# Performance work log

Hardware: AMD Instinct MI355X
Metric: run time of the kernel (lower is better)

The kernel has to match this reference:

```python
import jax, jax.numpy as jnp
import numpy as np


def setup_inputs() -> dict:
    key = jax.random.key(0)
    k1, k2 = jax.random.split(key)
    x = jax.random.normal(k1, (32, 64, 32, 32), dtype=jnp.float32)
    codebook = jax.random.normal(k2, (2048, 64), dtype=jnp.float32)
    return {"x": x, "codebook": codebook}


def reference(x, codebook):
    B, C, H, W = x.shape
    # (B, C, H, W) -> (B*H*W, C) channels-last flatten
    xf = jnp.transpose(x, (0, 2, 3, 1)).reshape(-1, C)
    d2 = (jnp.sum(xf * xf, axis=-1, keepdims=True)
          + jnp.sum(codebook * codebook, axis=-1)[None, :]
          - 2.0 * jnp.einsum('nc,kc->nk', xf, codebook))
    idx = jnp.argmin(d2, axis=-1)            # (B*H*W,)
    quant = codebook[idx]                    # (B*H*W, C)
    commitment_loss = jnp.mean((jax.lax.stop_gradient(quant) - xf) ** 2)
    codebook_loss = jnp.mean((quant - jax.lax.stop_gradient(xf)) ** 2)
    # Straight-through estimator
    quant_ste = xf + jax.lax.stop_gradient(quant - xf)
    quant_out = jnp.transpose(quant_ste.reshape(B, H, W, C), (0, 3, 1, 2))
    min_encoding_indices = idx.reshape(B, H, W)
    return quant_out, codebook_loss, commitment_loss, min_encoding_indices
```

## Files before the change

kernel.cpp:

```cpp
#include <hip/hip_runtime.h>

#define NROWS    32768
#define KENT     2048
#define OUT_Q_SZ 2097152
#define N_ELEMS  2097152.0f
#define THRG     1e-4f
#define KLO      0.0009765625f

typedef _Float16 f16x8  __attribute__((ext_vector_type(8)));
typedef float    f32x16 __attribute__((ext_vector_type(16)));

#define WS_EN    1024
#define WS_ENH   9216
#define WS_LIST  20480
#define WS_CBH   262144
#define WS_CBL   524288

__global__ __launch_bounds__(256) void vq_prep_kernel(
    const float* __restrict__ cb, float* __restrict__ ws)
{
    const int unit = blockIdx.x * 256 + threadIdx.x;
    if (unit == 0) { ws[0] = 0.0f; ((unsigned*)ws)[1] = 0u; ((unsigned*)ws)[2] = 0u; }

    const int gm = unit >> 8, ks = (unit >> 6) & 3, l = unit & 63;
    const int e  = gm * 32 + (l & 31);
    const int ch = ks * 16 + ((l >> 5) << 3);
    float4 v0 = *(const float4*)(cb + e * 64 + ch);
    float4 v1 = *(const float4*)(cb + e * 64 + ch + 4);
    float vv[8] = {v0.x,v0.y,v0.z,v0.w, v1.x,v1.y,v1.z,v1.w};
    f16x8 h, lo;
#pragma unroll
    for (int j = 0; j < 8; ++j) {
        _Float16 hi = (_Float16)vv[j];
        float r = (vv[j] - (float)hi) * 1024.0f;
        h[j] = hi; lo[j] = (_Float16)r;
    }
    *(f16x8*)((_Float16*)((char*)ws + WS_CBH) + (size_t)unit * 8) = h;
    *(f16x8*)((_Float16*)((char*)ws + WS_CBL) + (size_t)unit * 8) = lo;

    if (unit < KENT) {
        const float4* row = (const float4*)(cb + unit * 64);
        float s = 0.0f;
#pragma unroll
        for (int i = 0; i < 16; ++i) {
            float4 v = row[i];
            s += v.x * v.x + v.y * v.y + v.z * v.z + v.w * v.w;
        }
        *((float*)((char*)ws + WS_EN) + unit) = s;
        int ein = unit & 31;
        int half = (ein >> 2) & 1;
        int r = (ein & 3) + ((ein >> 3) << 2);
        *((float*)((char*)ws + WS_ENH) + (unit & ~31) + half * 16 + r) = -0.5f * s;
    }
}

__global__ __launch_bounds__(512, 4) void vq_main_kernel(
    const float* __restrict__ x, const float* __restrict__ cb,
    float* __restrict__ ws, float* __restrict__ out_q,
    float* __restrict__ out_idx)
{
    __shared__ float lds_x[64 * 68];
    __shared__ float enh_s[2048];
    __shared__ float mb1[64 * 4], mb2[64 * 4];
    __shared__ int   mbi[64 * 4];
    __shared__ int   idx_s[64], flag_s[64];
    __shared__ float wp[8];

    const _Float16* cbh  = (const _Float16*)((char*)ws + WS_CBH);
    const _Float16* cbl  = (const _Float16*)((char*)ws + WS_CBL);
    const float*    enhp = (const float*)((char*)ws + WS_ENH);
    unsigned* cnt  = (unsigned*)ws + 1;
    unsigned* list = (unsigned*)((char*)ws + WS_LIST);

    const int tid = threadIdx.x, bid = blockIdx.x;
    const int n0  = bid * 64;
    const int b   = n0 >> 10;
    const int hw0 = n0 & 1023;
    const float* xg = x + b * 65536 + hw0;

    {
        int c = tid >> 3, seg = tid & 7;
        float4 a0 = *(const float4*)(xg + c * 1024 + seg * 8);
        float4 a1 = *(const float4*)(xg + c * 1024 + seg * 8 + 4);
        *(float4*)(&lds_x[c * 68 + seg * 8])     = a0;
        *(float4*)(&lds_x[c * 68 + seg * 8 + 4]) = a1;
    }
#pragma unroll
    for (int i = tid; i < 2048; i += 512) enh_s[i] = enhp[i];
    __syncthreads();

    const int l   = tid & 63;
    const int wv  = tid >> 6;
    const int rgp = wv >> 2;
    const int eq  = wv & 3;
    const int r0  = rgp * 32;

    f16x8 bh[4], bl[4];
#pragma unroll
    for (int ks = 0; ks < 4; ++ks) {
        f16x8 h, lo;
#pragma unroll
        for (int j = 0; j < 8; ++j) {
            int ch = ks * 16 + ((l >> 5) << 3) + j;
            float f = lds_x[ch * 68 + r0 + (l & 31)];
            _Float16 hi = (_Float16)f;
            float r = (f - (float)hi) * 1024.0f;
            h[j] = hi; lo[j] = (_Float16)r;
        }
        bh[ks] = h; bl[ks] = lo;
    }

    float m1[4], m2[4]; int bx[4];
#pragma unroll
    for (int t = 0; t < 4; ++t) { m1[t] = -3.4e38f; m2[t] = -3.4e38f; bx[t] = 0; }

#pragma unroll 2
    for (int m = 0; m < 16; ++m) {
        const int gm = eq * 16 + m;
        const _Float16* ap = cbh + ((size_t)(gm * 4) * 64 + l) * 8;
        const _Float16* lp = cbl + ((size_t)(gm * 4) * 64 + l) * 8;
        f16x8 ah0 = *(const f16x8*)(ap);
        f16x8 ah1 = *(const f16x8*)(ap + 512);
        f16x8 ah2 = *(const f16x8*)(ap + 1024);
        f16x8 ah3 = *(const f16x8*)(ap + 1536);
        f16x8 al0 = *(const f16x8*)(lp);
        f16x8 al1 = *(const f16x8*)(lp + 512);
        f16x8 al2 = *(const f16x8*)(lp + 1024);
        f16x8 al3 = *(const f16x8*)(lp + 1536);

        f32x16 aA;
        {
            const float4* ep4 = (const float4*)(&enh_s[eq * 512 + m * 32 + ((l >> 5) << 4)]);
            float4 q0 = ep4[0], q1 = ep4[1], q2 = ep4[2], q3 = ep4[3];
            aA[0]=q0.x; aA[1]=q0.y; aA[2]=q0.z; aA[3]=q0.w;
            aA[4]=q1.x; aA[5]=q1.y; aA[6]=q1.z; aA[7]=q1.w;
            aA[8]=q2.x; aA[9]=q2.y; aA[10]=q2.z; aA[11]=q2.w;
            aA[12]=q3.x; aA[13]=q3.y; aA[14]=q3.z; aA[15]=q3.w;
        }
        f32x16 cA = {0.f,0.f,0.f,0.f,0.f,0.f,0.f,0.f,0.f,0.f,0.f,0.f,0.f,0.f,0.f,0.f};

        aA = __builtin_amdgcn_mfma_f32_32x32x16_f16(ah0, bh[0], aA, 0, 0, 0);
        cA = __builtin_amdgcn_mfma_f32_32x32x16_f16(ah0, bl[0], cA, 0, 0, 0);
        aA = __builtin_amdgcn_mfma_f32_32x32x16_f16(ah1, bh[1], aA, 0, 0, 0);
        cA = __builtin_amdgcn_mfma_f32_32x32x16_f16(ah1, bl[1], cA, 0, 0, 0);
        aA = __builtin_amdgcn_mfma_f32_32x32x16_f16(ah2, bh[2], aA, 0, 0, 0);
        cA = __builtin_amdgcn_mfma_f32_32x32x16_f16(ah2, bl[2], cA, 0, 0, 0);
        aA = __builtin_amdgcn_mfma_f32_32x32x16_f16(ah3, bh[3], aA, 0, 0, 0);
        cA = __builtin_amdgcn_mfma_f32_32x32x16_f16(ah3, bl[3], cA, 0, 0, 0);
        cA = __builtin_amdgcn_mfma_f32_32x32x16_f16(al0, bh[0], cA, 0, 0, 0);
        cA = __builtin_amdgcn_mfma_f32_32x32x16_f16(al1, bh[1], cA, 0, 0, 0);
        cA = __builtin_amdgcn_mfma_f32_32x32x16_f16(al2, bh[2], cA, 0, 0, 0);
        cA = __builtin_amdgcn_mfma_f32_32x32x16_f16(al3, bh[3], cA, 0, 0, 0);

        const int ebl = eq * 512 + m * 32 + ((l >> 5) << 2);
#pragma unroll
        for (int r = 0; r < 16; ++r) {
            int t = r >> 2;
            int ent = ebl + ((r >> 2) << 3) + (r & 3);
            float gA = fmaf(cA[r], KLO, aA[r]);
            bool  tA = gA > m1[t];
            m2[t] = __builtin_amdgcn_fmed3f(gA, m1[t], m2[t]);
            m1[t] = fmaxf(gA, m1[t]);
            bx[t] = tA ? ent : bx[t];
        }
    }

    {
        float v1 = m1[0], v2 = m2[0]; int ix = bx[0];
#pragma unroll
        for (int t = 1; t < 4; ++t) {
            bool gt = (m1[t] > v1) || (m1[t] == v1 && bx[t] < ix);
            float loser = gt ? v1 : m1[t];
            v1 = gt ? m1[t] : v1;
            ix = gt ? bx[t] : ix;
            v2 = fmaxf(loser, fmaxf(v2, m2[t]));
        }
        float o1 = __shfl_xor(v1, 32, 64);
        float o2 = __shfl_xor(v2, 32, 64);
        int   oi = __shfl_xor(ix, 32, 64);
        bool gt = (o1 > v1) || (o1 == v1 && oi < ix);
        float loser = gt ? v1 : o1;
        v1 = gt ? o1 : v1; ix = gt ? oi : ix;
        v2 = fmaxf(loser, fmaxf(v2, o2));
        if (l < 32) {
            int row = r0 + l;
            mb1[row * 4 + eq] = v1;
            mb2[row * 4 + eq] = v2;
            mbi[row * 4 + eq] = ix;
        }
    }
    __syncthreads();

    if (tid < 64) {
        float v1 = -3.4e38f, v2 = -3.4e38f; int ix = 0;
#pragma unroll
        for (int q = 0; q < 4; ++q) {
            float o1 = mb1[tid * 4 + q];
            float o2 = mb2[tid * 4 + q];
            int   oi = mbi[tid * 4 + q];
            bool gt = (o1 > v1) || (o1 == v1 && oi < ix);
            float loser = gt ? v1 : o1;
            v1 = gt ? o1 : v1; ix = gt ? oi : ix;
            v2 = fmaxf(loser, fmaxf(v2, o2));
        }
        out_idx[n0 + tid] = (float)ix;
        int fl = (v1 - v2) <= THRG;
        idx_s[tid] = ix; flag_s[tid] = fl;
        if (fl) { unsigned p = atomicAdd(cnt, 1u); list[p] = n0 + tid; }
    }
    __syncthreads();

    float lsum = 0.0f;
#pragma unroll
    for (int it = 0; it < 8; ++it) {
        int e = it * 512 + tid;
        int c = e >> 6, r = e & 63;
        float q  = cb[idx_s[r] * 64 + c];
        float xv = lds_x[c * 68 + r];
        out_q[(b << 16) + (c << 10) + hw0 + r] = xv + (q - xv);
        float df = q - xv;
        lsum += flag_s[r] ? 0.0f : df * df;
    }
#pragma unroll
    for (int mm = 1; mm < 64; mm <<= 1) lsum += __shfl_xor(lsum, mm, 64);
    if (l == 0) wp[wv] = lsum;
    __syncthreads();
    if (tid == 0) {
        float s = 0.0f;
#pragma unroll
        for (int w = 0; w < 8; ++w) s += wp[w];
        atomicAdd(ws, s);
    }
}

__global__ __launch_bounds__(256) void vq_fallback_kernel(
    const float* __restrict__ x, const float* __restrict__ cb,
    float* __restrict__ ws, float* __restrict__ out_q, float* __restrict__ out_idx)
{
    __shared__ float x_s[64];
    __shared__ float rd[256];
    __shared__ int   ri[256];
    __shared__ unsigned lastflag;

    const float* en = (const float*)((char*)ws + WS_EN);
    const unsigned F = *(const unsigned*)((char*)ws + 4);
    const unsigned* list = (const unsigned*)((char*)ws + WS_LIST);
    unsigned* done = (unsigned*)ws + 2;
    const int t = threadIdx.x;

    for (unsigned li = blockIdx.x; li < F; li += gridDim.x) {
        int row = list[li];
        int b = row >> 10, hw = row & 1023;
        if (t < 64) x_s[t] = x[(b << 16) + (t << 10) + hw];
        __syncthreads();

        float best = 3.4e38f; int bi = 0;
#pragma unroll 1
        for (int i = 0; i < 8; ++i) {
            int e = i * 256 + t;
            float dot = 0.0f;
#pragma unroll
            for (int c4 = 0; c4 < 16; ++c4) {
                float4 cv = *(const float4*)(cb + e * 64 + c4 * 4);
                float4 xv = *(const float4*)&x_s[c4 * 4];
                dot += cv.x * xv.x + cv.y * xv.y + cv.z * xv.z + cv.w * xv.w;
            }
            float d = en[e] - 2.0f * dot;
            if (d < best) { best = d; bi = e; }
        }
        rd[t] = best; ri[t] = bi;
        __syncthreads();
        for (int s = 128; s > 0; s >>= 1) {
            if (t < s) {
                bool lt = (rd[t + s] < rd[t]) ||
                          (rd[t + s] == rd[t] && ri[t + s] < ri[t]);
                if (lt) { rd[t] = rd[t + s]; ri[t] = ri[t + s]; }
            }
            __syncthreads();
        }
        int ix = ri[0];
        if (t == 0) out_idx[row] = (float)ix;
        if (t < 64) {
            float q = cb[ix * 64 + t];
            float xv = x_s[t];
            out_q[(b << 16) + (t << 10) + hw] = xv + (q - xv);
            float df = q - xv;
            float ls = df * df;
#pragma unroll
            for (int mm = 1; mm < 64; mm <<= 1) ls += __shfl_xor(ls, mm, 64);
            if (t == 0) atomicAdd(ws, ls);
        }
        __syncthreads();
    }

    __threadfence();
    if (t == 0) lastflag = atomicAdd(done, 1u);
    __syncthreads();
    if (lastflag == gridDim.x - 1 && t == 0) {
        float m = (*(volatile float*)ws) * (1.0f / N_ELEMS);
        out_q[OUT_Q_SZ]     = m;
        out_q[OUT_Q_SZ + 1] = m;
    }
}

extern "C" void kernel_launch(void* const* d_in, const int* in_sizes, int n_in,
                              void* d_out, int out_size, void* d_ws, size_t ws_size,
                              hipStream_t stream) {
    const float* x  = (const float*)d_in[0];
    const float* cb = (const float*)d_in[1];
    float* out  = (float*)d_out;
    float* ws   = (float*)d_ws;
    float* oidx = out + OUT_Q_SZ + 2;

    vq_prep_kernel<<<64, 256, 0, stream>>>(cb, ws);
    vq_main_kernel<<<512, 512, 0, stream>>>(x, cb, ws, out, oidx);
    vq_fallback_kernel<<<64, 256, 0, stream>>>(x, cb, ws, out, oidx);
}
```

Before: 80.60 us.

## Split codebook across blocks, stage codebook via LDS DMA, separate epilogue kernel

The main kernel now covers 128 rows per block and one quarter of the codebook. Codebook fp16 hi/lo tiles are loaded into double-buffered LDS with global_load_lds, so all four waves share them instead of each wave loading them from global memory. Per-quarter partial max/second-max/index results go to workspace, and a new epilogue kernel merges them, writes the quantized output and accumulates the loss. This cuts global codebook traffic and raises the number of blocks, at the cost of an extra launch, workspace round-trips, re-reading x from global memory, and a block-wide barrier on every iteration.

New measurement: 81.81 us. Within noise of the previous version (+1.5%).

```diff
diff --git a/kernel.cpp b/kernel.cpp
--- a/kernel.cpp
+++ b/kernel.cpp
@@ -15,6 +15,9 @@
 #define WS_LIST  20480
 #define WS_CBH   262144
 #define WS_CBL   524288
+#define WS_PM1   1048576
+#define WS_PIX   1572864
+#define WS_PM2   2097152
 
 __global__ __launch_bounds__(256) void vq_prep_kernel(
     const float* __restrict__ cb, float* __restrict__ ws)
@@ -54,46 +57,38 @@
     }
 }
 
-__global__ __launch_bounds__(512, 4) void vq_main_kernel(
-    const float* __restrict__ x, const float* __restrict__ cb,
-    float* __restrict__ ws, float* __restrict__ out_q,
-    float* __restrict__ out_idx)
+__global__ __launch_bounds__(256, 3) void vq_main_kernel(
+    const float* __restrict__ x, float* __restrict__ ws)
 {
-    __shared__ float lds_x[64 * 68];
-    __shared__ float enh_s[2048];
-    __shared__ float mb1[64 * 4], mb2[64 * 4];
-    __shared__ int   mbi[64 * 4];
-    __shared__ int   idx_s[64], flag_s[64];
-    __shared__ float wp[8];
-
-    const _Float16* cbh  = (const _Float16*)((char*)ws + WS_CBH);
-    const _Float16* cbl  = (const _Float16*)((char*)ws + WS_CBL);
-    const float*    enhp = (const float*)((char*)ws + WS_ENH);
-    unsigned* cnt  = (unsigned*)ws + 1;
-    unsigned* list = (unsigned*)((char*)ws + WS_LIST);
+    __shared__ char  uni[33792];
+    __shared__ float enh_s[512];
+
+    const char*  cbh  = (const char*)ws + WS_CBH;
+    const char*  cbl  = (const char*)ws + WS_CBL;
+    const float* enhp = (const float*)((char*)ws + WS_ENH);
+    float* pm1 = (float*)((char*)ws + WS_PM1);
+    int*   pix = (int*)  ((char*)ws + WS_PIX);
+    float* pm2 = (float*)((char*)ws + WS_PM2);
 
     const int tid = threadIdx.x, bid = blockIdx.x;
-    const int n0  = bid * 64;
+    const int rowgrp  = bid >> 2;
+    const int quarter = bid & 3;
+    const int n0  = rowgrp * 128;
     const int b   = n0 >> 10;
     const int hw0 = n0 & 1023;
     const float* xg = x + b * 65536 + hw0;
-
-    {
-        int c = tid >> 3, seg = tid & 7;
-        float4 a0 = *(const float4*)(xg + c * 1024 + seg * 8);
-        float4 a1 = *(const float4*)(xg + c * 1024 + seg * 8 + 4);
-        *(float4*)(&lds_x[c * 68 + seg * 8])     = a0;
-        *(float4*)(&lds_x[c * 68 + seg * 8 + 4]) = a1;
-    }
-#pragma unroll
-    for (int i = tid; i < 2048; i += 512) enh_s[i] = enhp[i];
-    __syncthreads();
-
-    const int l   = tid & 63;
-    const int wv  = tid >> 6;
-    const int rgp = wv >> 2;
-    const int eq  = wv & 3;
-    const int r0  = rgp * 32;
+    const int l  = tid & 63;
+    const int wv = tid >> 6;
+
+    float* lds_x = (float*)uni;
+#pragma unroll
+    for (int it = 0; it < 8; ++it) {
+        int f = it * 256 + tid;
+        int c = f >> 5, seg = f & 31;
+        float4 v = *(const float4*)(xg + c * 1024 + seg * 4);
+        *(float4*)(&lds_x[c * 132 + seg * 4]) = v;
+    }
+    __syncthreads();
 
     f16x8 bh[4], bl[4];
 #pragma unroll
@@ -102,13 +97,32 @@
 #pragma unroll
         for (int j = 0; j < 8; ++j) {
             int ch = ks * 16 + ((l >> 5) << 3) + j;
-            float f = lds_x[ch * 68 + r0 + (l & 31)];
+            float f = lds_x[ch * 132 + wv * 32 + (l & 31)];
             _Float16 hi = (_Float16)f;
             float r = (f - (float)hi) * 1024.0f;
             h[j] = hi; lo[j] = (_Float16)r;
         }
         bh[ks] = h; bl[ks] = lo;
     }
+    __syncthreads();
+
+    for (int i = tid; i < 512; i += 256) enh_s[i] = enhp[quarter * 512 + i];
+
+#define STAGE(MM, SLOT) do {                                                   \
+    const char* gh_ = cbh + (size_t)(quarter * 16 + (MM)) * 4096 + tid * 16;   \
+    const char* gl_ = cbl + (size_t)(quarter * 16 + (MM)) * 4096 + tid * 16;   \
+    __builtin_amdgcn_global_load_lds(                                          \
+        (const __attribute__((address_space(1))) void*)gh_,                    \
+        (__attribute__((address_space(3))) void*)&uni[(SLOT) * 8192 + wv * 1024],          \
+        16, 0, 0);                                                             \
+    __builtin_amdgcn_global_load_lds(                                          \
+        (const __attribute__((address_space(1))) void*)gl_,                    \
+        (__attribute__((address_space(3))) void*)&uni[(SLOT) * 8192 + 4096 + wv * 1024],   \
+        16, 0, 0);                                                             \
+} while (0)
+
+    STAGE(0, 0);
+    __syncthreads();
 
     float m1[4], m2[4]; int bx[4];
 #pragma unroll
@@ -116,21 +130,21 @@
 
 #pragma unroll 2
     for (int m = 0; m < 16; ++m) {
-        const int gm = eq * 16 + m;
-        const _Float16* ap = cbh + ((size_t)(gm * 4) * 64 + l) * 8;
-        const _Float16* lp = cbl + ((size_t)(gm * 4) * 64 + l) * 8;
-        f16x8 ah0 = *(const f16x8*)(ap);
-        f16x8 ah1 = *(const f16x8*)(ap + 512);
-        f16x8 ah2 = *(const f16x8*)(ap + 1024);
-        f16x8 ah3 = *(const f16x8*)(ap + 1536);
-        f16x8 al0 = *(const f16x8*)(lp);
-        f16x8 al1 = *(const f16x8*)(lp + 512);
-        f16x8 al2 = *(const f16x8*)(lp + 1024);
-        f16x8 al3 = *(const f16x8*)(lp + 1536);
+        if (m < 15) STAGE(m + 1, (m + 1) & 1);
+
+        const char* sb = &uni[(m & 1) * 8192];
+        f16x8 ah0 = *(const f16x8*)(sb + (l) * 16);
+        f16x8 ah1 = *(const f16x8*)(sb + (64 + l) * 16);
+        f16x8 ah2 = *(const f16x8*)(sb + (128 + l) * 16);
+        f16x8 ah3 = *(const f16x8*)(sb + (192 + l) * 16);
+        f16x8 al0 = *(const f16x8*)(sb + 4096 + (l) * 16);
+        f16x8 al1 = *(const f16x8*)(sb + 4096 + (64 + l) * 16);
+        f16x8 al2 = *(const f16x8*)(sb + 4096 + (128 + l) * 16);
+        f16x8 al3 = *(const f16x8*)(sb + 4096 + (192 + l) * 16);
 
         f32x16 aA;
         {
-            const float4* ep4 = (const float4*)(&enh_s[eq * 512 + m * 32 + ((l >> 5) << 4)]);
+            const float4* ep4 = (const float4*)(&enh_s[m * 32 + ((l >> 5) << 4)]);
             float4 q0 = ep4[0], q1 = ep4[1], q2 = ep4[2], q3 = ep4[3];
             aA[0]=q0.x; aA[1]=q0.y; aA[2]=q0.z; aA[3]=q0.w;
             aA[4]=q1.x; aA[5]=q1.y; aA[6]=q1.z; aA[7]=q1.w;
@@ -152,18 +166,20 @@
         cA = __builtin_amdgcn_mfma_f32_32x32x16_f16(al2, bh[2], cA, 0, 0, 0);
         cA = __builtin_amdgcn_mfma_f32_32x32x16_f16(al3, bh[3], cA, 0, 0, 0);
 
-        const int ebl = eq * 512 + m * 32 + ((l >> 5) << 2);
+        const int ebl = quarter * 512 + m * 32 + ((l >> 5) << 2);
 #pragma unroll
         for (int r = 0; r < 16; ++r) {
             int t = r >> 2;
             int ent = ebl + ((r >> 2) << 3) + (r & 3);
-            float gA = fmaf(cA[r], KLO, aA[r]);
-            bool  tA = gA > m1[t];
-            m2[t] = __builtin_amdgcn_fmed3f(gA, m1[t], m2[t]);
-            m1[t] = fmaxf(gA, m1[t]);
-            bx[t] = tA ? ent : bx[t];
-        }
-    }
+            float g = fmaf(cA[r], KLO, aA[r]);
+            bool  gt = g > m1[t];
+            m2[t] = __builtin_amdgcn_fmed3f(g, m1[t], m2[t]);
+            m1[t] = fmaxf(g, m1[t]);
+            bx[t] = gt ? ent : bx[t];
+        }
+        __syncthreads();
+    }
+#undef STAGE
 
     {
         float v1 = m1[0], v2 = m2[0]; int ix = bx[0];
@@ -183,54 +199,67 @@
         v1 = gt ? o1 : v1; ix = gt ? oi : ix;
         v2 = fmaxf(loser, fmaxf(v2, o2));
         if (l < 32) {
-            int row = r0 + l;
-            mb1[row * 4 + eq] = v1;
-            mb2[row * 4 + eq] = v2;
-            mbi[row * 4 + eq] = ix;
-        }
-    }
-    __syncthreads();
-
-    if (tid < 64) {
-        float v1 = -3.4e38f, v2 = -3.4e38f; int ix = 0;
+            int row = n0 + wv * 32 + l;
+            pm1[quarter * NROWS + row] = v1;
+            pix[quarter * NROWS + row] = ix;
+            pm2[quarter * NROWS + row] = v2;
+        }
+    }
+}
+
+__global__ __launch_bounds__(256) void vq_epilogue_kernel(
+    const float* __restrict__ x, const float* __restrict__ cb,
+    float* __restrict__ ws, float* __restrict__ out_q, float* __restrict__ out_idx)
+{
+    __shared__ int   idx_s[64], flag_s[64];
+    __shared__ float wp[4];
+
+    const float* pm1 = (const float*)((char*)ws + WS_PM1);
+    const int*   pix = (const int*)  ((char*)ws + WS_PIX);
+    const float* pm2 = (const float*)((char*)ws + WS_PM2);
+    unsigned* cnt  = (unsigned*)ws + 1;
+    unsigned* list = (unsigned*)((char*)ws + WS_LIST);
+
+    const int t = threadIdx.x;
+    const int base = blockIdx.x * 64;
+    const int b = base >> 10, hw0 = base & 1023;
+
+    if (t < 64) {
+        int row = base + t;
+        float v1 = -3.4e38f, v2 = -3.4e38f; int ix = 0x7fffffff;
 #pragma unroll
         for (int q = 0; q < 4; ++q) {
-            float o1 = mb1[tid * 4 + q];
-            float o2 = mb2[tid * 4 + q];
-            int   oi = mbi[tid * 4 + q];
+            float o1 = pm1[q * NROWS + row];
+            int   oi = pix[q * NROWS + row];
+            float o2 = pm2[q * NROWS + row];
             bool gt = (o1 > v1) || (o1 == v1 && oi < ix);
             float loser = gt ? v1 : o1;
             v1 = gt ? o1 : v1; ix = gt ? oi : ix;
             v2 = fmaxf(loser, fmaxf(v2, o2));
         }
-        out_idx[n0 + tid] = (float)ix;
+        out_idx[row] = (float)ix;
         int fl = (v1 - v2) <= THRG;
-        idx_s[tid] = ix; flag_s[tid] = fl;
-        if (fl) { unsigned p = atomicAdd(cnt, 1u); list[p] = n0 + tid; }
+        idx_s[t] = ix; flag_s[t] = fl;
+        if (fl) { unsigned p = atomicAdd(cnt, 1u); list[p] = row; }
     }
     __syncthreads();
 
     float lsum = 0.0f;
 #pragma unroll
-    for (int it = 0; it < 8; ++it) {
-        int e = it * 512 + tid;
+    for (int it = 0; it < 16; ++it) {
+        int e = it * 256 + t;
         int c = e >> 6, r = e & 63;
         float q  = cb[idx_s[r] * 64 + c];
-        float xv = lds_x[c * 68 + r];
+        float xv = x[(b << 16) + (c << 10) + hw0 + r];
         out_q[(b << 16) + (c << 10) + hw0 + r] = xv + (q - xv);
         float df = q - xv;
         lsum += flag_s[r] ? 0.0f : df * df;
     }
 #pragma unroll
     for (int mm = 1; mm < 64; mm <<= 1) lsum += __shfl_xor(lsum, mm, 64);
-    if (l == 0) wp[wv] = lsum;
-    __syncthreads();
-    if (tid == 0) {
-        float s = 0.0f;
-#pragma unroll
-        for (int w = 0; w < 8; ++w) s += wp[w];
-        atomicAdd(ws, s);
-    }
+    if ((t & 63) == 0) wp[t >> 6] = lsum;
+    __syncthreads();
+    if (t == 0) atomicAdd(ws, wp[0] + wp[1] + wp[2] + wp[3]);
 }
 
 __global__ __launch_bounds__(256) void vq_fallback_kernel(
@@ -313,6 +342,7 @@
     float* oidx = out + OUT_Q_SZ + 2;
 
     vq_prep_kernel<<<64, 256, 0, stream>>>(cb, ws);
-    vq_main_kernel<<<512, 512, 0, stream>>>(x, cb, ws, out, oidx);
+    vq_main_kernel<<<1024, 256, 0, stream>>>(x, ws);
+    vq_epilogue_kernel<<<512, 256, 0, stream>>>(x, cb, ws, out, oidx);
     vq_fallback_kernel<<<64, 256, 0, stream>>>(x, cb, ws, out, oidx);
 }
```
